# Kernel optimization log

Measured on AMD Instinct MI355X. Metric: run time of the kernel, lower is better.

The kernel has to match this reference:

```python
import jax, jax.numpy as jnp
import numpy as np
import math

B, S, D = 4, 4096, 1024
NUM_HEADS = 8  # hardcoded in the original via `// 8` and view(..., 8, head_dim)
HEAD_DIM = D // NUM_HEADS


def setup_inputs() -> dict:
    key = jax.random.key(0)
    ks = jax.random.split(key, 11)
    s = 1.0 / math.sqrt(D)
    inp = {
        "input_seq": jax.random.normal(ks[0], (B, S, D), dtype=jnp.float32),
        # Linear weights stored as [in, out] (y = x @ W + b), matching nn.Linear math
        "Wq": jax.random.uniform(ks[1], (D, D), jnp.float32, -s, s),
        "bq": jax.random.uniform(ks[2], (D,), jnp.float32, -s, s),
        "Wk": jax.random.uniform(ks[3], (D, D), jnp.float32, -s, s),
        "bk": jax.random.uniform(ks[4], (D,), jnp.float32, -s, s),
        "Wv": jax.random.uniform(ks[5], (D, D), jnp.float32, -s, s),
        "bv": jax.random.uniform(ks[6], (D,), jnp.float32, -s, s),
        "W1": jax.random.uniform(ks[7], (D, D), jnp.float32, -s, s),
        "b1": jax.random.uniform(ks[8], (D,), jnp.float32, -s, s),
        "W2": jax.random.uniform(ks[9], (D, D), jnp.float32, -s, s),
        "b2": jax.random.uniform(ks[10], (D,), jnp.float32, -s, s),
    }
    return inp


def reference(input_seq, Wq, bq, Wk, bk, Wv, bv, W1, b1, W2, b2):
    # QKV projections (query=key=input_seq in self-attention)
    q = input_seq @ Wq + bq  # [B,S,D]
    k = input_seq @ Wk + bk
    v = input_seq @ Wv + bv

    # Faithful to the original: view(B, S, 8, head_dim) with NO transpose,
    # so attention is computed over the 8 heads within each token position.
    q = q.reshape(B, S, NUM_HEADS, HEAD_DIM)
    k = k.reshape(B, S, NUM_HEADS, HEAD_DIM)
    v = v.reshape(B, S, NUM_HEADS, HEAD_DIM)

    # scores[b,s,h,t] = q[b,s,h,:] . k[b,s,t,:] / sqrt(head_dim)  -> [B,S,8,8]
    scores = jnp.einsum("bshd,bstd->bsht", q, k) / jnp.sqrt(jnp.float32(HEAD_DIM))
    # dropout on scores before softmax: identity at inference
    attn_weights = jax.nn.softmax(scores, axis=-1)  # [B,S,8,8]

    out = jnp.einsum("bsht,bstd->bshd", attn_weights, v).reshape(B, S, D)
    # dropout on attn_output: identity at inference

    # FFN: Linear -> ReLU -> Linear (no residual / layernorm in the original)
    ff = jnp.maximum(out @ W1 + b1, 0.0) @ W2 + b2
    return ff, attn_weights
```

## Files before the change

### kernel.cpp

```cpp
#include <hip/hip_runtime.h>
#include <hip/hip_bf16.h>


#define DI __device__ __forceinline__

typedef __bf16 bf16raw;
typedef bf16raw bf16x8 __attribute__((ext_vector_type(8)));
typedef float floatx4 __attribute__((ext_vector_type(4)));

DI unsigned short f2bf(float f) {
    __hip_bfloat16 h = __float2bfloat16(f);
    return *reinterpret_cast<unsigned short*>(&h);
}

DI void async16(unsigned short* lds, const unsigned short* g) {
    __builtin_amdgcn_global_load_lds(
        (const __attribute__((address_space(1))) void*)g,
        (__attribute__((address_space(3))) void*)lds,
        16, 0, 0);
}

template <typename T> DI T cvt_out(float v);
template <> DI float cvt_out<float>(float v) { return v; }
template <> DI unsigned short cvt_out<unsigned short>(float v) { return f2bf(v); }

template <typename OutT, bool RELU>
__global__ __launch_bounds__(256)
void gemm_bt_kernel(const unsigned short* __restrict__ A,
                    const unsigned short* __restrict__ Bt,
                    const float* __restrict__ bias,
                    OutT* __restrict__ C,
                    int M, int N, int K)
{
    constexpr int BM = 128, BN = 128, BK = 64;
    __shared__ unsigned short As[BM * BK];
    __shared__ unsigned short Bs[BN * BK];

    const int tid  = threadIdx.x;
    const int wave = tid >> 6;
    const int lane = tid & 63;
    const int quad = lane >> 4;
    const int l16  = lane & 15;
    const int sw7  = l16 & 7;

    const int m0 = blockIdx.y * BM;
    const int n0 = blockIdx.x * BN;
    const int wm = (wave >> 1) * 64;
    const int wn = (wave & 1) * 64;

    floatx4 acc[4][4];
    const floatx4 zero = {0.f, 0.f, 0.f, 0.f};
#pragma unroll
    for (int i = 0; i < 4; i++)
#pragma unroll
        for (int j = 0; j < 4; j++) acc[i][j] = zero;

    const int rA = lane >> 3;
    const int kA = (((lane & 7) ^ rA) * 8);
    const unsigned short* aS[4];
    const unsigned short* bS[4];
    unsigned short* aD[4];
    unsigned short* bD[4];
#pragma unroll
    for (int c = 0; c < 4; c++) {
        const int row = wave * 32 + c * 8 + rA;
        aS[c] = A  + (size_t)(m0 + row) * K + kA;
        bS[c] = Bt + (size_t)(n0 + row) * K + kA;
        aD[c] = &As[wave * 2048 + c * 512];
        bD[c] = &Bs[wave * 2048 + c * 512];
    }

    for (int kt = 0; kt < K; kt += BK) {
        __syncthreads();
#pragma unroll
        for (int c = 0; c < 4; c++) {
            async16(aD[c], aS[c] + kt);
            async16(bD[c], bS[c] + kt);
        }
        __syncthreads();

#pragma unroll
        for (int s = 0; s < 2; s++) {
            bf16x8 af[4], bfr[4];
            const int slot = ((s * 4 + quad) ^ sw7) * 8;
#pragma unroll
            for (int i = 0; i < 4; i++)
                af[i] = *reinterpret_cast<const bf16x8*>(
                    &As[(wm + i * 16 + l16) * BK + slot]);
#pragma unroll
            for (int j = 0; j < 4; j++)
                bfr[j] = *reinterpret_cast<const bf16x8*>(
                    &Bs[(wn + j * 16 + l16) * BK + slot]);
#pragma unroll
            for (int i = 0; i < 4; i++)
#pragma unroll
                for (int j = 0; j < 4; j++)
                    acc[i][j] = __builtin_amdgcn_mfma_f32_16x16x32_bf16(
                        af[i], bfr[j], acc[i][j], 0, 0, 0);
        }
    }

#pragma unroll
    for (int j = 0; j < 4; j++) {
        const int col = n0 + wn + j * 16 + l16;
        const float bv = bias[col];
#pragma unroll
        for (int i = 0; i < 4; i++) {
            const int rbase = m0 + wm + i * 16 + quad * 4;
#pragma unroll
            for (int r = 0; r < 4; r++) {
                float v = acc[i][j][r] + bv;
                if (RELU) v = fmaxf(v, 0.f);
                C[(size_t)(rbase + r) * N + col] = cvt_out<OutT>(v);
            }
        }
    }
}

__global__ void cast_f32_to_bf16(const float* __restrict__ src,
                                 unsigned short* __restrict__ dst, int n4) {
    int i = blockIdx.x * blockDim.x + threadIdx.x;
    if (i < n4) {
        float4 v = reinterpret_cast<const float4*>(src)[i];
        ushort4 o = { f2bf(v.x), f2bf(v.y), f2bf(v.z), f2bf(v.w) };
        reinterpret_cast<ushort4*>(dst)[i] = o;
    }
}

struct WPack {
    const float* src[5];
    unsigned short* dst[5];
};
__global__ void transpose_cast_all(WPack p) {
    __shared__ float tile[32][33];
    const float* W = p.src[blockIdx.z];
    unsigned short* Wt = p.dst[blockIdx.z];
    const int n0 = blockIdx.x * 32, k0 = blockIdx.y * 32;
    const int tx = threadIdx.x, ty = threadIdx.y;
#pragma unroll
    for (int i = 0; i < 32; i += 8)
        tile[ty + i][tx] = W[(size_t)(k0 + ty + i) * 1024 + n0 + tx];
    __syncthreads();
#pragma unroll
    for (int i = 0; i < 32; i += 8)
        Wt[(size_t)(n0 + ty + i) * 1024 + k0 + tx] = f2bf(tile[tx][ty + i]);
}

__global__ void concat_bias(const float* __restrict__ bq,
                            const float* __restrict__ bk,
                            const float* __restrict__ bv,
                            float* __restrict__ dst) {
    int i = blockIdx.x * blockDim.x + threadIdx.x;
    const float* s = (i < 1024) ? bq : ((i < 2048) ? bk : bv);
    dst[i] = s[i & 1023];
}

DI float dot8(unsigned a, unsigned b, float acc) {
    union { unsigned u; float f; } al, ah, bl, bh;
    al.u = a << 16; ah.u = a & 0xffff0000u;
    bl.u = b << 16; bh.u = b & 0xffff0000u;
    return acc + al.f * bl.f + ah.f * bh.f;
}

__global__ __launch_bounds__(256)
void attention_kernel(const unsigned short* __restrict__ qkv,
                      unsigned short* __restrict__ out_bf,
                      float* __restrict__ attn_w)
{
    __shared__ unsigned short sqkv[4][3072];
    __shared__ float sw[4][64];
    const int tid  = threadIdx.x;
    const int wave = tid >> 6;
    const int lane = tid & 63;
    const int m    = blockIdx.x * 4 + wave;

    {
        const uint4* src = reinterpret_cast<const uint4*>(qkv + (size_t)m * 3072);
        uint4* dst = reinterpret_cast<uint4*>(&sqkv[wave][0]);
#pragma unroll
        for (int i = 0; i < 6; i++) dst[lane + 64 * i] = src[lane + 64 * i];
    }
    __syncthreads();

    {
        const int h = lane >> 3, t = lane & 7;
        const uint2* q8 = reinterpret_cast<const uint2*>(&sqkv[wave][h * 128]);
        const uint2* k8 = reinterpret_cast<const uint2*>(&sqkv[wave][1024 + t * 128]);
        float dot = 0.f;
#pragma unroll
        for (int d = 0; d < 32; d++) {
            uint2 a = q8[d], b = k8[d];
            dot = dot8(a.x, b.x, dot);
            dot = dot8(a.y, b.y, dot);
        }
        float score = dot * 0.08838834764831843f;
        float mx = score;
#pragma unroll
        for (int o = 1; o < 8; o <<= 1) mx = fmaxf(mx, __shfl_xor(mx, o, 8));
        float e = __expf(score - mx);
        float sum = e;
#pragma unroll
        for (int o = 1; o < 8; o <<= 1) sum += __shfl_xor(sum, o, 8);
        float w = e / sum;
        sw[wave][lane] = w;
        attn_w[(size_t)m * 64 + lane] = w;
    }
    __syncthreads();

    {
        const int h  = lane >> 3;
        const int d0 = (lane & 7) * 16;
        float acc[16];
#pragma unroll
        for (int i = 0; i < 16; i++) acc[i] = 0.f;
#pragma unroll
        for (int t = 0; t < 8; t++) {
            const float w = sw[wave][h * 8 + t];
            const uint4* v8 = reinterpret_cast<const uint4*>(
                &sqkv[wave][2048 + t * 128 + d0]);
            uint4 v0 = v8[0], v1 = v8[1];
            unsigned vv[8] = { v0.x, v0.y, v0.z, v0.w, v1.x, v1.y, v1.z, v1.w };
#pragma unroll
            for (int i = 0; i < 8; i++) {
                union { unsigned u; float f; } lo, hi;
                lo.u = vv[i] << 16; hi.u = vv[i] & 0xffff0000u;
                acc[i * 2]     += w * lo.f;
                acc[i * 2 + 1] += w * hi.f;
            }
        }
        unsigned o[8];
#pragma unroll
        for (int i = 0; i < 8; i++)
            o[i] = (unsigned)f2bf(acc[i * 2]) | ((unsigned)f2bf(acc[i * 2 + 1]) << 16);
        uint4* dst = reinterpret_cast<uint4*>(out_bf + (size_t)m * 1024 + lane * 16);
        dst[0] = make_uint4(o[0], o[1], o[2], o[3]);
        dst[1] = make_uint4(o[4], o[5], o[6], o[7]);
    }
}

extern "C" void kernel_launch(void* const* d_in, const int* in_sizes, int n_in,
                              void* d_out, int out_size, void* d_ws, size_t ws_size,
                              hipStream_t stream) {
    const float* x  = (const float*)d_in[0];
    const float* Wq = (const float*)d_in[1];
    const float* bq = (const float*)d_in[2];
    const float* Wk = (const float*)d_in[3];
    const float* bk = (const float*)d_in[4];
    const float* Wv = (const float*)d_in[5];
    const float* bv = (const float*)d_in[6];
    const float* W1 = (const float*)d_in[7];
    const float* b1 = (const float*)d_in[8];
    const float* W2 = (const float*)d_in[9];
    const float* b2 = (const float*)d_in[10];

    constexpr int D = 1024;
    constexpr int M = 4 * 4096;
    constexpr size_t XN = (size_t)M * D;

    float* ff_out   = (float*)d_out;
    float* attn_out = (float*)d_out + XN;

    char* ws = (char*)d_ws;
    size_t off = 0;
    auto alloc = [&](size_t bytes) -> char* {
        char* p = ws + off;
        off += (bytes + 255) & ~(size_t)255;
        return p;
    };
    unsigned short* Xbf   = (unsigned short*)alloc(XN * 2);
    unsigned short* Wtqkv = (unsigned short*)alloc((size_t)3 * D * D * 2);
    unsigned short* Wt1   = (unsigned short*)alloc((size_t)D * D * 2);
    unsigned short* Wt2   = (unsigned short*)alloc((size_t)D * D * 2);
    float*          bqkv  = (float*)alloc(3 * D * 4);
    unsigned short* outbf = (unsigned short*)alloc(XN * 2);
    unsigned short* hbf   = (unsigned short*)alloc(XN * 2);
    unsigned short* qkv   = (unsigned short*)alloc((size_t)M * 3 * D * 2);

    cast_f32_to_bf16<<<(int)(XN / 4 / 256), 256, 0, stream>>>(x, Xbf, (int)(XN / 4));
    WPack p;
    p.src[0] = Wq; p.dst[0] = Wtqkv;
    p.src[1] = Wk; p.dst[1] = Wtqkv + (size_t)D * D;
    p.src[2] = Wv; p.dst[2] = Wtqkv + (size_t)2 * D * D;
    p.src[3] = W1; p.dst[3] = Wt1;
    p.src[4] = W2; p.dst[4] = Wt2;
    transpose_cast_all<<<dim3(32, 32, 5), dim3(32, 8), 0, stream>>>(p);
    concat_bias<<<12, 256, 0, stream>>>(bq, bk, bv, bqkv);

    gemm_bt_kernel<unsigned short, false><<<dim3(3 * D / 128, M / 128), 256, 0, stream>>>(
        Xbf, Wtqkv, bqkv, qkv, M, 3 * D, D);
    attention_kernel<<<M / 4, 256, 0, stream>>>(qkv, outbf, attn_out);

    gemm_bt_kernel<unsigned short, true><<<dim3(D / 128, M / 128), 256, 0, stream>>>(
        outbf, Wt1, b1, hbf, M, D, D);
    gemm_bt_kernel<float, false><<<dim3(D / 128, M / 128), 256, 0, stream>>>(
        hbf, Wt2, b2, ff_out, M, D, D);
}
```

Measured before the change: 418.6 us.

## Remap GEMM blocks per XCD and make GEMM dimensions compile-time

Remaps GEMM block indices so that consecutive blocks, which the hardware distributes round-robin across the 8 XCDs, give each XCD a contiguous band of M rows. The aim is better L2 reuse of A tiles within each XCD. K and N become template constants, the per-chunk pointer arrays become a single base pointer with computed offsets to cut register use, and launch bounds request 3 blocks per CU. The remapping assumes gridDim.y is divisible by 8 and that the grid shapes are fixed.

```diff
diff --git a/kernel.cpp b/kernel.cpp
--- a/kernel.cpp
+++ b/kernel.cpp
@@ -24,13 +24,12 @@
 template <> DI float cvt_out<float>(float v) { return v; }
 template <> DI unsigned short cvt_out<unsigned short>(float v) { return f2bf(v); }
 
-template <typename OutT, bool RELU>
-__global__ __launch_bounds__(256)
+template <int K, int N, int GX, typename OutT, bool RELU>
+__global__ __launch_bounds__(256, 3)
 void gemm_bt_kernel(const unsigned short* __restrict__ A,
                     const unsigned short* __restrict__ Bt,
                     const float* __restrict__ bias,
-                    OutT* __restrict__ C,
-                    int M, int N, int K)
+                    OutT* __restrict__ C)
 {
     constexpr int BM = 128, BN = 128, BK = 64;
     __shared__ unsigned short As[BM * BK];
@@ -43,8 +42,14 @@
     const int l16  = lane & 15;
     const int sw7  = l16 & 7;
 
-    const int m0 = blockIdx.y * BM;
-    const int n0 = blockIdx.x * BN;
+    const int g   = blockIdx.x + GX * blockIdx.y;
+    const int xcd = g & 7;
+    const int t   = g >> 3;
+    const int bx  = t % GX;
+    const int by  = t / GX + (gridDim.y >> 3) * xcd;
+
+    const int m0 = by * BM;
+    const int n0 = bx * BN;
     const int wm = (wave >> 1) * 64;
     const int wn = (wave & 1) * 64;
 
@@ -57,25 +62,17 @@
 
     const int rA = lane >> 3;
     const int kA = (((lane & 7) ^ rA) * 8);
-    const unsigned short* aS[4];
-    const unsigned short* bS[4];
-    unsigned short* aD[4];
-    unsigned short* bD[4];
-#pragma unroll
-    for (int c = 0; c < 4; c++) {
-        const int row = wave * 32 + c * 8 + rA;
-        aS[c] = A  + (size_t)(m0 + row) * K + kA;
-        bS[c] = Bt + (size_t)(n0 + row) * K + kA;
-        aD[c] = &As[wave * 2048 + c * 512];
-        bD[c] = &Bs[wave * 2048 + c * 512];
-    }
+    const unsigned short* aBase = A  + (size_t)(m0 + wave * 32 + rA) * K + kA;
+    const unsigned short* bBase = Bt + (size_t)(n0 + wave * 32 + rA) * K + kA;
+    unsigned short* aD = &As[wave * 2048];
+    unsigned short* bD = &Bs[wave * 2048];
 
     for (int kt = 0; kt < K; kt += BK) {
         __syncthreads();
 #pragma unroll
         for (int c = 0; c < 4; c++) {
-            async16(aD[c], aS[c] + kt);
-            async16(bD[c], bS[c] + kt);
+            async16(aD + c * 512, aBase + c * 8 * K + kt);
+            async16(bD + c * 512, bBase + c * 8 * K + kt);
         }
         __syncthreads();
 
@@ -286,12 +283,12 @@
     transpose_cast_all<<<dim3(32, 32, 5), dim3(32, 8), 0, stream>>>(p);
     concat_bias<<<12, 256, 0, stream>>>(bq, bk, bv, bqkv);
 
-    gemm_bt_kernel<unsigned short, false><<<dim3(3 * D / 128, M / 128), 256, 0, stream>>>(
-        Xbf, Wtqkv, bqkv, qkv, M, 3 * D, D);
+    gemm_bt_kernel<D, 3 * D, 24, unsigned short, false>
+        <<<dim3(24, 128), 256, 0, stream>>>(Xbf, Wtqkv, bqkv, qkv);
     attention_kernel<<<M / 4, 256, 0, stream>>>(qkv, outbf, attn_out);
 
-    gemm_bt_kernel<unsigned short, true><<<dim3(D / 128, M / 128), 256, 0, stream>>>(
-        outbf, Wt1, b1, hbf, M, D, D);
-    gemm_bt_kernel<float, false><<<dim3(D / 128, M / 128), 256, 0, stream>>>(
-        hbf, Wt2, b2, ff_out, M, D, D);
-}
+    gemm_bt_kernel<D, D, 8, unsigned short, true>
+        <<<dim3(8, 128), 256, 0, stream>>>(outbf, Wt1, b1, hbf);
+    gemm_bt_kernel<D, D, 8, float, false>
+        <<<dim3(8, 128), 256, 0, stream>>>(hbf, Wt2, b2, ff_out);
+}
```

After: 397.0 us. 1.05x faster.
